# Kernel tuning notes

Hardware: AMD Instinct MI355X
Metric: run time of the kernel (lower is better)

The kernel has to match this reference:

```python
import jax, jax.numpy as jnp
import numpy as np

DIM = 1024

def setup_inputs() -> dict:
    key = jax.random.key(0)
    k1, k2 = jax.random.split(key)
    X = jax.random.normal(k1, (4, 4096, DIM), dtype=jnp.float32)
    # nn.Linear(dim, 3*dim): weight [3*dim, dim], bias [3*dim]
    W = jax.random.normal(k2, (3 * DIM, DIM), dtype=jnp.float32) * (1.0 / np.sqrt(DIM))
    b = jnp.zeros((3 * DIM,), dtype=jnp.float32)
    return {"X": X, "W": W, "b": b}

def reference(X, W, b):
    dim = X.shape[-1]
    # fused QKV projection: [B,S,3D]
    QKV = jnp.einsum('bsd,ed->bse', X, W) + b
    Q, K, V = jnp.split(QKV, 3, axis=-1)
    scale = 1.0 / jnp.sqrt(jnp.asarray(dim, X.dtype))
    scores = jnp.einsum('bqd,bkd->bqk', Q, K) * scale  # [B,S,S]
    attn = jax.nn.softmax(scores, axis=-1)
    return jnp.einsum('bqk,bkd->bqd', attn, V)
```

## Files before the change

kernel.cpp:

```cpp
#include <hip/hip_runtime.h>
#include <cstdint>

typedef unsigned short u16;
typedef __attribute__((ext_vector_type(8))) short bf16x8;
typedef __attribute__((ext_vector_type(4))) float f32x4;

#define DIM   1024
#define BATCH 4
#define SEQ   4096
#define E3    3072
#define MTOT  (BATCH*SEQ)

__device__ __forceinline__ u16 f2bf(float x) {
    union { float f; unsigned u; } v; v.f = x;
    unsigned r = v.u + 0x7FFFu + ((v.u >> 16) & 1u);
    return (u16)(r >> 16);
}

__device__ __forceinline__ void gl16(const void* g, void* l) {
    __builtin_amdgcn_global_load_lds(
        (const __attribute__((address_space(1))) void*)g,
        (__attribute__((address_space(3))) void*)l, 16, 0, 0);
}

__device__ __forceinline__ void gemm256(
    const u16* __restrict__ A, int sA,
    const u16* __restrict__ B, int sB,
    int K, int m0, int n0,
    u16* lds, f32x4 acc[8][4])
{
    const int t   = threadIdx.x;
    const int w   = t >> 6, L = t & 63;
    const int rL  = L & 15, kq = L >> 4;
    const int qa  = 2*w;
    const int ia0 = 8*(w>>2);
    const int jb0 = 4*(w&3);

    const size_t ga0 = (size_t)(m0 + qa*16 + rL)*sA + kq*8;
    const size_t ga1 = ga0 + (size_t)16*sA;
    const size_t gb0 = (size_t)(n0 + qa*16 + rL)*sB + kq*8;
    const size_t gb1 = gb0 + (size_t)16*sB;

    const int NT = K >> 5;
    bf16x8 av[8], bv[4];

#define STAGE_A(tile) { const size_t k0=(size_t)(tile)*32; \
    u16* sb = lds + ((tile)&3)*16384; \
    gl16(A + ga0 + k0, sb + qa*512); \
    gl16(A + ga1 + k0, sb + qa*512 + 512); }
#define STAGE_B(tile) { const size_t k0=(size_t)(tile)*32; \
    u16* sb = lds + ((tile)&3)*16384; \
    gl16(B + gb0 + k0, sb + 8192 + qa*512); \
    gl16(B + gb1 + k0, sb + 8192 + qa*512 + 512); }

#define FEN   __builtin_amdgcn_sched_barrier(0)
#define BARR  __builtin_amdgcn_s_barrier()
#define VMW(n) asm volatile("s_waitcnt vmcnt(" #n ")")
#define NOWAIT ((void)0)

#define PH0(tile, DOSTAGE) { \
    const u16* sb = lds + ((tile)&3)*16384; \
    _Pragma("unroll") \
    for (int i = 0; i < 4; ++i) av[i] = *(const bf16x8*)&sb[(ia0+i)*512 + L*8]; \
    _Pragma("unroll") \
    for (int j = 0; j < 4; ++j) bv[j] = *(const bf16x8*)&sb[8192 + (jb0+j)*512 + L*8]; \
    if (DOSTAGE) STAGE_A((tile)+3); \
    FEN; BARR; FEN; \
    __builtin_amdgcn_s_setprio(1); \
    _Pragma("unroll") \
    for (int i = 0; i < 4; ++i) \
        _Pragma("unroll") \
        for (int j = 0; j < 4; ++j) \
            acc[i][j] = __builtin_amdgcn_mfma_f32_16x16x32_bf16(av[i], bv[j], acc[i][j], 0,0,0); \
    __builtin_amdgcn_s_setprio(0); \
    FEN; BARR; }

#define PH1(tile, DOSTAGE, WAIT) { \
    const u16* sb = lds + ((tile)&3)*16384; \
    _Pragma("unroll") \
    for (int i = 0; i < 4; ++i) av[4+i] = *(const bf16x8*)&sb[(ia0+4+i)*512 + L*8]; \
    if (DOSTAGE) STAGE_B((tile)+3); \
    FEN; BARR; FEN; \
    __builtin_amdgcn_s_setprio(1); \
    _Pragma("unroll") \
    for (int i = 0; i < 4; ++i) \
        _Pragma("unroll") \
        for (int j = 0; j < 4; ++j) \
            acc[4+i][j] = __builtin_amdgcn_mfma_f32_16x16x32_bf16(av[4+i], bv[j], acc[4+i][j], 0,0,0); \
    __builtin_amdgcn_s_setprio(0); \
    FEN; WAIT; FEN; BARR; }

    STAGE_A(0); STAGE_B(0);
    STAGE_A(1); STAGE_B(1);
    STAGE_A(2); STAGE_B(2);
    FEN; VMW(8); FEN; BARR;

    for (int tt = 0; tt < NT-3; ++tt) {
        PH0(tt, 1);
        PH1(tt, 1, VMW(8));
    }
    PH0(NT-3, 0); PH1(NT-3, 0, VMW(4));
    PH0(NT-2, 0); PH1(NT-2, 0, VMW(0));
    PH0(NT-1, 0); PH1(NT-1, 0, NOWAIT);

#undef STAGE_A
#undef STAGE_B
#undef PH0
#undef PH1
#undef FEN
#undef BARR
#undef VMW
#undef NOWAIT
}

__global__ __launch_bounds__(256)
void cvt_bf16(const float* __restrict__ x, u16* __restrict__ y) {
    size_t i = ((size_t)blockIdx.x*256 + threadIdx.x)*4;
    float4 v = *(const float4*)&x[i];
    ushort4 h;
    h.x = f2bf(v.x); h.y = f2bf(v.y); h.z = f2bf(v.z); h.w = f2bf(v.w);
    *(ushort4*)&y[i] = h;
}

__global__ __launch_bounds__(512,2)
void gemm_qkv(const u16* __restrict__ Xbf, const u16* __restrict__ Wbf,
              const float* __restrict__ bias,
              u16* __restrict__ Qh, u16* __restrict__ Kh,
              u16* __restrict__ Vth)
{
    __shared__ __align__(16) u16 lds[65536];
    f32x4 acc[8][4];
    #pragma unroll
    for (int i=0;i<8;++i)
        #pragma unroll
        for (int j=0;j<4;++j) acc[i][j] = (f32x4){0.f,0.f,0.f,0.f};

    const int F = blockIdx.y*12 + blockIdx.x;
    const int c = F & 7, s = F >> 3;
    const int mrow = c*8 + (s & 7);
    const int ncol = s >> 3;
    const int m0 = mrow*256, n0 = ncol*256;
    gemm256(Xbf, DIM, Wbf, DIM, DIM, m0, n0, lds, acc);

    const int t = threadIdx.x, w = t>>6, L = t&63;
    const int wm = 128*(w>>2), wn = 64*(w&3);
    const int cl = L&15, rq = (L>>4)*4;
    const int region = n0 >> 10;
    const float qscale = 0.03125f;

    if (region < 2) {
        u16* Dst = region ? Kh : Qh;
        const float fs = region ? 1.0f : qscale;
        #pragma unroll
        for (int j = 0; j < 4; ++j) {
            float bc = bias[n0 + wn + j*16 + cl];
            #pragma unroll
            for (int i = 0; i < 8; ++i)
                #pragma unroll
                for (int r = 0; r < 4; ++r)
                    acc[i][j][r] = (acc[i][j][r] + bc)*fs;
        }
        const int d0 = (n0 & 1023) + wn;
        #pragma unroll
        for (int p = 0; p < 2; ++p) {
            const int nt0 = 2*p, nt1 = 2*p+1;
            #pragma unroll
            for (int i = 0; i < 8; ++i) {
                int row0 = m0 + wm + i*16 + rq;
                int bi = row0 >> 12, s0 = row0 & (SEQ-1);
                #pragma unroll
                for (int r = 0; r < 4; ++r) {
                    float v0 = acc[i][nt0][r], v1 = acc[i][nt1][r];
                    float x0 = __shfl_xor(v0, 1, 64);
                    float x1 = __shfl_xor(v1, 1, 64);
                    unsigned wv; int colb;
                    if ((cl & 1) == 0) {
                        wv   = (unsigned)f2bf(v0) | ((unsigned)f2bf(x0) << 16);
                        colb = nt0*16 + cl;
                    } else {
                        wv   = (unsigned)f2bf(x1) | ((unsigned)f2bf(v1) << 16);
                        colb = nt1*16 + (cl-1);
                    }
                    size_t idx = ((size_t)bi*SEQ + s0 + r)*DIM + d0 + colb;
                    *(unsigned*)&Dst[idx] = wv;
                }
            }
        }
    } else {
        #pragma unroll
        for (int j = 0; j < 4; ++j) {
            int col = n0 + wn + j*16 + cl;
            float bc = bias[col];
            int d = col & (DIM-1);
            #pragma unroll
            for (int i = 0; i < 8; ++i) {
                int row0 = m0 + wm + i*16 + rq;
                int bi = row0 >> 12, s0 = row0 & (SEQ-1);
                ushort4 hv;
                hv.x = f2bf(acc[i][j][0] + bc);
                hv.y = f2bf(acc[i][j][1] + bc);
                hv.z = f2bf(acc[i][j][2] + bc);
                hv.w = f2bf(acc[i][j][3] + bc);
                size_t base = ((size_t)bi*DIM + d)*SEQ + s0;
                *(ushort4*)&Vth[base] = hv;
            }
        }
    }
}

__global__ __launch_bounds__(512,2)
void gemm_scores(const u16* __restrict__ Qh, const u16* __restrict__ Kh,
                 u16* __restrict__ S0, u16* __restrict__ S1,
                 u16* __restrict__ S2, u16* __restrict__ S3)
{
    __shared__ __align__(16) u16 lds[65536];
    f32x4 acc[8][4];
    #pragma unroll
    for (int i=0;i<8;++i)
        #pragma unroll
        for (int j=0;j<4;++j) acc[i][j] = (f32x4){0.f,0.f,0.f,0.f};

    const int F = (blockIdx.z*16 + blockIdx.y)*16 + blockIdx.x;
    const int c = F & 7, s = F >> 3;
    const int st = s >> 5, v = s & 31;
    const int bz   = c >> 1;
    const int mrow = (c&1)*8 + (st>>1)*4 + (v>>3);
    const int ncol = (st&1)*8 + (v&7);
    const size_t qo = (size_t)bz*SEQ*DIM;
    const int m0 = mrow*256, n0 = ncol*256;
    gemm256(Qh + qo, DIM, Kh + qo, DIM, DIM, m0, n0, lds, acc);

    u16* Sb = (bz == 0) ? S0 : (bz == 1) ? S1 : (bz == 2) ? S2 : S3;
    const int t = threadIdx.x, w = t>>6, L = t&63;
    const int wm = 128*(w>>2), wn = 64*(w&3);
    const int cl = L&15, rq = (L>>4)*4;
    #pragma unroll
    for (int p = 0; p < 2; ++p) {
        const int nt0 = 2*p, nt1 = 2*p+1;
        #pragma unroll
        for (int i = 0; i < 8; ++i) {
            int row0 = m0 + wm + i*16 + rq;
            #pragma unroll
            for (int r = 0; r < 4; ++r) {
                float v0 = acc[i][nt0][r], v1 = acc[i][nt1][r];
                float x0 = __shfl_xor(v0, 1, 64);
                float x1 = __shfl_xor(v1, 1, 64);
                unsigned wv; int colb;
                if ((cl & 1) == 0) {
                    wv   = (unsigned)f2bf(v0) | ((unsigned)f2bf(x0) << 16);
                    colb = nt0*16 + cl;
                } else {
                    wv   = (unsigned)f2bf(x1) | ((unsigned)f2bf(v1) << 16);
                    colb = nt1*16 + (cl-1);
                }
                *(unsigned*)&Sb[(size_t)(row0 + r)*SEQ + n0 + wn + colb] = wv;
            }
        }
    }
}

__global__ __launch_bounds__(256)
void softmax_pack(u16* __restrict__ S0, u16* __restrict__ S1,
                  u16* __restrict__ S2, u16* __restrict__ S3)
{
    __shared__ float red[4];
    const int t = threadIdx.x, L = t & 63, w = t >> 6;
    const int gr = blockIdx.x, bz = gr >> 12, rr = gr & (SEQ-1);
    u16* Sb = (bz == 0) ? S0 : (bz == 1) ? S1 : (bz == 2) ? S2 : S3;
    u16* row = Sb + (size_t)rr*SEQ;

    float v[16];
    float m = -1e30f;
    #pragma unroll
    for (int j = 0; j < 2; ++j) {
        ushort4 x0 = *(const ushort4*)&row[t*8 + j*2048];
        ushort4 x1 = *(const ushort4*)&row[t*8 + j*2048 + 4];
        union { unsigned u; float f; } c;
        c.u = (unsigned)x0.x << 16; v[8*j+0] = c.f;
        c.u = (unsigned)x0.y << 16; v[8*j+1] = c.f;
        c.u = (unsigned)x0.z << 16; v[8*j+2] = c.f;
        c.u = (unsigned)x0.w << 16; v[8*j+3] = c.f;
        c.u = (unsigned)x1.x << 16; v[8*j+4] = c.f;
        c.u = (unsigned)x1.y << 16; v[8*j+5] = c.f;
        c.u = (unsigned)x1.z << 16; v[8*j+6] = c.f;
        c.u = (unsigned)x1.w << 16; v[8*j+7] = c.f;
    }
    #pragma unroll
    for (int i = 0; i < 16; ++i) m = fmaxf(m, v[i]);
    #pragma unroll
    for (int off = 32; off; off >>= 1) m = fmaxf(m, __shfl_xor(m, off, 64));
    if (L == 0) red[w] = m;
    __syncthreads();
    m = fmaxf(fmaxf(red[0],red[1]), fmaxf(red[2],red[3]));

    float s = 0.f;
    #pragma unroll
    for (int i = 0; i < 16; ++i) { v[i] = __expf(v[i] - m); s += v[i]; }
    #pragma unroll
    for (int off = 32; off; off >>= 1) s += __shfl_xor(s, off, 64);
    __syncthreads();
    if (L == 0) red[w] = s;
    __syncthreads();
    s = red[0]+red[1]+red[2]+red[3];
    const float inv = 1.0f / s;

    #pragma unroll
    for (int j = 0; j < 2; ++j) {
        ushort4 h0, h1;
        h0.x = f2bf(v[8*j+0]*inv); h0.y = f2bf(v[8*j+1]*inv);
        h0.z = f2bf(v[8*j+2]*inv); h0.w = f2bf(v[8*j+3]*inv);
        h1.x = f2bf(v[8*j+4]*inv); h1.y = f2bf(v[8*j+5]*inv);
        h1.z = f2bf(v[8*j+6]*inv); h1.w = f2bf(v[8*j+7]*inv);
        *(ushort4*)&row[t*8 + j*2048]     = h0;
        *(ushort4*)&row[t*8 + j*2048 + 4] = h1;
    }
}

__global__ __launch_bounds__(512,2)
void gemm_pv(const u16* __restrict__ P0, const u16* __restrict__ P1,
             const u16* __restrict__ P2, const u16* __restrict__ P3,
             const u16* __restrict__ Vth,
             float* __restrict__ O0, float* __restrict__ O1,
             float* __restrict__ O2, float* __restrict__ O3)
{
    __shared__ __align__(16) u16 lds[65536];
    f32x4 acc[8][4];
    #pragma unroll
    for (int i=0;i<8;++i)
        #pragma unroll
        for (int j=0;j<4;++j) acc[i][j] = (f32x4){0.f,0.f,0.f,0.f};

    const int F = (blockIdx.z*16 + blockIdx.y)*4 + blockIdx.x;
    const int c = F & 7, s = F >> 3;
    const int bz   = c >> 1;
    const int mrow = (c&1)*8 + (s>>2);
    const int ncol = s & 3;
    const u16* Pb = (bz == 0) ? P0 : (bz == 1) ? P1 : (bz == 2) ? P2 : P3;
    float*     Ob = (bz == 0) ? O0 : (bz == 1) ? O1 : (bz == 2) ? O2 : O3;
    const int m0 = mrow*256, n0 = ncol*256;
    gemm256(Pb, SEQ, Vth + (size_t)bz*DIM*SEQ, SEQ, SEQ, m0, n0, lds, acc);

    const int t = threadIdx.x, w = t>>6, L = t&63;
    const int wm = 128*(w>>2), wn = 64*(w&3);
    const int cl = L&15, rq = (L>>4)*4;
    #pragma unroll
    for (int j = 0; j < 4; ++j) {
        int col = n0 + wn + j*16 + cl;
        #pragma unroll
        for (int i = 0; i < 8; ++i) {
            int row0 = m0 + wm + i*16 + rq;
            #pragma unroll
            for (int r = 0; r < 4; ++r)
                Ob[(size_t)(row0 + r)*DIM + col] = acc[i][j][r];
        }
    }
}

__global__ __launch_bounds__(256)
void copy_out(const float* __restrict__ src, float* __restrict__ dst)
{
    size_t i = ((size_t)blockIdx.x*256 + threadIdx.x)*4;
    *(float4*)&dst[i] = *(const float4*)&src[i];
}

extern "C" void kernel_launch(void* const* d_in, const int* in_sizes, int n_in,
                              void* d_out, int out_size, void* d_ws, size_t ws_size,
                              hipStream_t stream) {
    const float* X    = (const float*)d_in[0];
    const float* W    = (const float*)d_in[1];
    const float* bias = (const float*)d_in[2];
    float* out = (float*)d_out;

    const size_t MB = (size_t)1 << 20;
    if (ws_size < 192*MB) return;
    char* ws = (char*)d_ws;
    char* wo = (char*)d_out;
    u16* Qh  = (u16*)ws;
    u16* Kh  = (u16*)(ws + 32*MB);
    u16* Vth = (u16*)(ws + 64*MB);
    u16* S0  = (u16*)(ws + 96*MB);
    u16* S1  = (u16*)(ws + 128*MB);
    u16* S2  = (u16*)(ws + 160*MB);
    u16* Xbf = (u16*)wo;
    u16* Wbf = (u16*)(wo + 32*MB);
    u16* S3  = (u16*)(wo + 32*MB);
    float* O0 = (float*)wo;
    float* O1 = (float*)(wo + 16*MB);
    float* O2 = (float*)ws;
    float* O3 = (float*)(ws + 16*MB);

    cvt_bf16<<<MTOT*DIM/1024, 256, 0, stream>>>(X, Xbf);
    cvt_bf16<<<E3*DIM/1024,   256, 0, stream>>>(W, Wbf);

    gemm_qkv<<<dim3(E3/256, MTOT/256), 512, 0, stream>>>(
        Xbf, Wbf, bias, Qh, Kh, Vth);

    gemm_scores<<<dim3(SEQ/256, SEQ/256, BATCH), 512, 0, stream>>>(
        Qh, Kh, S0, S1, S2, S3);

    softmax_pack<<<MTOT, 256, 0, stream>>>(S0, S1, S2, S3);

    gemm_pv<<<dim3(DIM/256, SEQ/256, BATCH), 512, 0, stream>>>(
        S0, S1, S2, S3, Vth, O0, O1, O2, O3);

    copy_out<<<(32*MB/sizeof(float))/1024, 256, 0, stream>>>(
        (const float*)ws, out + 8*MB);
}
```

Before: 581.2 us.

## Restructure GEMM mainloop to K=64 double-buffered tiles with split A/B staging

Changes the shared GEMM core from four 32-wide K buffers (3-deep prefetch) to two 64-wide K buffers with double buffering. Loads are interleaved across four sub-phases, each pairing a half of the A or B tile prefetch with one block of MFMAs. This halves the number of outer iterations and changes the LDS layout and the barrier/waitcnt schedule. It aims to cut barrier and loop overhead per unit of compute, at the cost of shallower prefetch depth and more complex vmcnt bookkeeping, which risks race or latency exposure.

```diff
diff --git a/kernel.cpp b/kernel.cpp
--- a/kernel.cpp
+++ b/kernel.cpp
@@ -29,88 +29,83 @@
     int K, int m0, int n0,
     u16* lds, f32x4 acc[8][4])
 {
-    const int t   = threadIdx.x;
-    const int w   = t >> 6, L = t & 63;
+    const int tid = threadIdx.x;
+    const int w   = tid >> 6, L = tid & 63;
     const int rL  = L & 15, kq = L >> 4;
-    const int qa  = 2*w;
-    const int ia0 = 8*(w>>2);
-    const int jb0 = 4*(w&3);
-
-    const size_t ga0 = (size_t)(m0 + qa*16 + rL)*sA + kq*8;
-    const size_t ga1 = ga0 + (size_t)16*sA;
-    const size_t gb0 = (size_t)(n0 + qa*16 + rL)*sB + kq*8;
-    const size_t gb1 = gb0 + (size_t)16*sB;
-
-    const int NT = K >> 5;
-    bf16x8 av[8], bv[4];
-
-#define STAGE_A(tile) { const size_t k0=(size_t)(tile)*32; \
-    u16* sb = lds + ((tile)&3)*16384; \
-    gl16(A + ga0 + k0, sb + qa*512); \
-    gl16(A + ga1 + k0, sb + qa*512 + 512); }
-#define STAGE_B(tile) { const size_t k0=(size_t)(tile)*32; \
-    u16* sb = lds + ((tile)&3)*16384; \
-    gl16(B + gb0 + k0, sb + 8192 + qa*512); \
-    gl16(B + gb1 + k0, sb + 8192 + qa*512 + 512); }
-
-#define FEN   __builtin_amdgcn_sched_barrier(0)
-#define BARR  __builtin_amdgcn_s_barrier()
+    const int wg8 = (w>>2)*8;
+    const int jb4 = 4*(w&3);
+
+    const int mA = wg8 + (w&3);
+    const size_t gA  = (size_t)(m0 + mA*16 + rL)*sA + kq*8;
+    const size_t gAm = (size_t)64*sA;
+    const size_t gB0 = (size_t)(n0 + (2*w)*16 + rL)*sB + kq*8;
+    const size_t gB1 = gB0 + (size_t)16*sB;
+
+    const int ldsA  = (mA*2)*512 + L*8;
+    const int ldsB0 = 16384 + (2*w*2)*512 + L*8;
+    const int ldsB1 = 16384 + ((2*w+1)*2)*512 + L*8;
+
+    const int NT = K >> 6;
+    bf16x8 av[4], bv[4];
+
+#define FEN    __builtin_amdgcn_sched_barrier(0)
+#define BARR   __builtin_amdgcn_s_barrier()
 #define VMW(n) asm volatile("s_waitcnt vmcnt(" #n ")")
-#define NOWAIT ((void)0)
-
-#define PH0(tile, DOSTAGE) { \
-    const u16* sb = lds + ((tile)&3)*16384; \
+
+#define SAU(mh, tn) { u16* bn = lds + (((tn)&1)<<15); \
+    const size_t g = gA + (size_t)(mh)*gAm + (size_t)(tn)*64; \
+    gl16(A + g,      bn + ldsA + (mh)*4096); \
+    gl16(A + g + 32, bn + ldsA + (mh)*4096 + 512); }
+
+#define SBU(ks, tn) { u16* bn = lds + (((tn)&1)<<15); \
+    const size_t g = (size_t)(tn)*64 + (size_t)(ks)*32; \
+    gl16(B + gB0 + g, bn + ldsB0 + (ks)*512); \
+    gl16(B + gB1 + g, bn + ldsB1 + (ks)*512); }
+
+#define RD(mh, ks, tcur) { const u16* bc = lds + (((tcur)&1)<<15); \
     _Pragma("unroll") \
-    for (int i = 0; i < 4; ++i) av[i] = *(const bf16x8*)&sb[(ia0+i)*512 + L*8]; \
-    _Pragma("unroll") \
-    for (int j = 0; j < 4; ++j) bv[j] = *(const bf16x8*)&sb[8192 + (jb0+j)*512 + L*8]; \
-    if (DOSTAGE) STAGE_A((tile)+3); \
-    FEN; BARR; FEN; \
+    for (int i = 0; i < 4; ++i) \
+        av[i] = *(const bf16x8*)&bc[((wg8+(mh)*4+i)*2+(ks))*512 + L*8]; \
+    if ((mh) == 0) { \
+        _Pragma("unroll") \
+        for (int j = 0; j < 4; ++j) \
+            bv[j] = *(const bf16x8*)&bc[16384 + ((jb4+j)*2+(ks))*512 + L*8]; } }
+
+#define MM(mh) { \
     __builtin_amdgcn_s_setprio(1); \
     _Pragma("unroll") \
     for (int i = 0; i < 4; ++i) \
         _Pragma("unroll") \
         for (int j = 0; j < 4; ++j) \
-            acc[i][j] = __builtin_amdgcn_mfma_f32_16x16x32_bf16(av[i], bv[j], acc[i][j], 0,0,0); \
-    __builtin_amdgcn_s_setprio(0); \
-    FEN; BARR; }
-
-#define PH1(tile, DOSTAGE, WAIT) { \
-    const u16* sb = lds + ((tile)&3)*16384; \
-    _Pragma("unroll") \
-    for (int i = 0; i < 4; ++i) av[4+i] = *(const bf16x8*)&sb[(ia0+4+i)*512 + L*8]; \
-    if (DOSTAGE) STAGE_B((tile)+3); \
-    FEN; BARR; FEN; \
-    __builtin_amdgcn_s_setprio(1); \
-    _Pragma("unroll") \
-    for (int i = 0; i < 4; ++i) \
-        _Pragma("unroll") \
-        for (int j = 0; j < 4; ++j) \
-            acc[4+i][j] = __builtin_amdgcn_mfma_f32_16x16x32_bf16(av[4+i], bv[j], acc[4+i][j], 0,0,0); \
-    __builtin_amdgcn_s_setprio(0); \
-    FEN; WAIT; FEN; BARR; }
-
-    STAGE_A(0); STAGE_B(0);
-    STAGE_A(1); STAGE_B(1);
-    STAGE_A(2); STAGE_B(2);
-    FEN; VMW(8); FEN; BARR;
-
-    for (int tt = 0; tt < NT-3; ++tt) {
-        PH0(tt, 1);
-        PH1(tt, 1, VMW(8));
-    }
-    PH0(NT-3, 0); PH1(NT-3, 0, VMW(4));
-    PH0(NT-2, 0); PH1(NT-2, 0, VMW(0));
-    PH0(NT-1, 0); PH1(NT-1, 0, NOWAIT);
-
-#undef STAGE_A
-#undef STAGE_B
-#undef PH0
-#undef PH1
+            acc[(mh)*4+i][j] = __builtin_amdgcn_mfma_f32_16x16x32_bf16(av[i], bv[j], acc[(mh)*4+i][j], 0,0,0); \
+    __builtin_amdgcn_s_setprio(0); }
+
+    SAU(0,0); SBU(0,0); SAU(1,0); SBU(1,0);
+
+    for (int tt = 0; tt < NT-1; ++tt) {
+        FEN; VMW(4); BARR; FEN;
+        RD(0,0,tt); FEN; SAU(0,tt+1); FEN; MM(0);
+        FEN; VMW(4); BARR; FEN;
+        RD(1,0,tt); FEN; SBU(0,tt+1); FEN; MM(1);
+        FEN; VMW(4); BARR; FEN;
+        RD(0,1,tt); FEN; SAU(1,tt+1); FEN; MM(0);
+        FEN;
+        RD(1,1,tt); FEN; SBU(1,tt+1); FEN; MM(1);
+    }
+    {   const int tt = NT-1;
+        FEN; VMW(4); BARR; FEN; RD(0,0,tt); FEN; MM(0);
+        FEN; VMW(2); BARR; FEN; RD(1,0,tt); FEN; MM(1);
+        FEN; VMW(0); BARR; FEN; RD(0,1,tt); FEN; MM(0);
+        FEN;                    RD(1,1,tt); FEN; MM(1);
+    }
+
+#undef SAU
+#undef SBU
+#undef RD
+#undef MM
 #undef FEN
 #undef BARR
 #undef VMW
-#undef NOWAIT
 }
 
 __global__ __launch_bounds__(256)
```

Result: faster. 561.9 us (-3.3%).
